# Performance work log

Hardware: AMD Instinct MI355X
Metric: run time of the kernel (lower is better)

The kernel has to match this reference:

```python
import jax, jax.numpy as jnp
import numpy as np

G = 8          # grid_size
N = G * G      # 64 nodes
DEG = 17       # neighbors per node for 8x8 sudoku (2x4 boxes)
STEPS = 32
H = 96         # hidden_dim
E = 16         # embed_size
B = 16         # batch


def sudoku_edges():
    # row (7) + col (7) + 2x4 box (7) neighbors, set-union -> 17 per node
    idx = np.arange(N).reshape(G, G)
    nb = []
    for j in range(N):
        r, c = j // G, j % G
        br, bc = (r // 2) * 2, (c // 4) * 4
        s = set(idx[r, :].tolist()) | set(idx[:, c].tolist()) | set(idx[br:br + 2, bc:bc + 4].flatten().tolist())
        s.discard(j)
        nb.append(sorted(s))
    return np.asarray(nb, dtype=np.int32)  # [64, 17]


def setup_inputs() -> dict:
    key = jax.random.key(0)
    ks = jax.random.split(key, 16)
    sc = 0.05
    inp = {
        "x": jax.random.randint(ks[0], (B, G, G), 0, G + 1),            # given digits, 0 = blank
        "target": jax.random.randint(ks[1], (B, G, G), 0, G) + 1,       # solutions in 1..8
        "edges": jnp.asarray(sudoku_edges()),                            # [64, 17] int32
        "digit_emb": jax.random.normal(ks[2], (G + 1, E), jnp.float32) * sc,
        "row_emb": jax.random.normal(ks[3], (G, E), jnp.float32) * sc,
        "col_emb": jax.random.normal(ks[4], (G, E), jnp.float32) * sc,
        "in0_W": jax.random.normal(ks[5], (3 * E, H), jnp.float32) * sc,
        "in0_b": jnp.zeros((H,), jnp.float32),
        "in_Ws": jax.random.normal(ks[6], (3, H, H), jnp.float32) * sc,
        "in_bs": jnp.zeros((3, H), jnp.float32),
        "msg0_W": jax.random.normal(ks[7], (2 * H, H), jnp.float32) * sc,
        "msg0_b": jnp.zeros((H,), jnp.float32),
        "msg_Ws": jax.random.normal(ks[8], (3, H, H), jnp.float32) * sc,
        "msg_bs": jnp.zeros((3, H), jnp.float32),
        "W_ih": jax.random.normal(ks[9], (2 * H, 4 * H), jnp.float32) * sc,
        "W_hh": jax.random.normal(ks[10], (H, 4 * H), jnp.float32) * sc,
        "b_ih": jnp.zeros((4 * H,), jnp.float32),
        "b_hh": jnp.zeros((4 * H,), jnp.float32),
        "pred_W": jax.random.normal(ks[11], (H, G), jnp.float32) * sc,
        "pred_b": jnp.zeros((G,), jnp.float32),
    }
    return inp


def _mlp(z, W0, b0, Ws, bs):
    # Linear -> ReLU -> Linear -> ReLU -> Linear -> ReLU -> Linear (def_MLP)
    z = jax.nn.relu(z @ W0 + b0)
    z = jax.nn.relu(z @ Ws[0] + bs[0])
    z = jax.nn.relu(z @ Ws[1] + bs[1])
    return z @ Ws[2] + bs[2]


def reference(x, target, edges, digit_emb, row_emb, col_emb,
              in0_W, in0_b, in_Ws, in_bs,
              msg0_W, msg0_b, msg_Ws, msg_bs,
              W_ih, W_hh, b_ih, b_hh, pred_W, pred_b):
    bsz = x.shape[0]
    xf = x.reshape(bsz, N)
    tgt = target.reshape(bsz, N) - 1                      # labels 0..7

    de = digit_emb[xf]                                    # [B,64,E]
    re = row_emb[jnp.repeat(jnp.arange(G), G)]            # [64,E]
    ce = col_emb[jnp.tile(jnp.arange(G), G)]              # [64,E]
    feat = jnp.concatenate([de,
                            jnp.broadcast_to(re[None], (bsz, N, E)),
                            jnp.broadcast_to(ce[None], (bsz, N, E))], axis=-1)
    xin = _mlp(feat, in0_W, in0_b, in_Ws, in_bs)          # [B,64,H]

    h0 = jnp.zeros((bsz, N, H), jnp.float32)
    s0 = jnp.zeros((bsz * N, H), jnp.float32)

    def step(carry, _):
        h, s, loss = carry
        # gather-by-edge message passing
        h_edges = h[:, edges]                                             # [B,64,17,H]
        h_self = jnp.broadcast_to(h[:, :, None, :], (bsz, N, DEG, H))
        msg = _mlp(jnp.concatenate([h_edges, h_self], -1),
                   msg0_W, msg0_b, msg_Ws, msg_bs).sum(axis=2)            # [B,64,H]
        # LSTMCell update
        lstm_in = jnp.concatenate([msg, xin], -1).reshape(bsz * N, 2 * H)
        gates = lstm_in @ W_ih + b_ih + h.reshape(bsz * N, H) @ W_hh + b_hh
        i, f, g, o = jnp.split(gates, 4, axis=-1)
        s2 = jax.nn.sigmoid(f) * s + jax.nn.sigmoid(i) * jnp.tanh(g)
        h2 = (jax.nn.sigmoid(o) * jnp.tanh(s2)).reshape(bsz, N, H)
        # per-step prediction / loss / accuracy
        logp = jax.nn.log_softmax(h2 @ pred_W + pred_b, axis=-1)          # [B,64,8]
        pred = jnp.argmax(logp, axis=-1)
        acc = jnp.mean(jnp.all(pred == tgt, axis=1).astype(jnp.float32))
        loss_n = -jnp.sum(jnp.take_along_axis(logp, tgt[..., None], -1)) / (bsz * N)
        return (h2, s2, loss + loss_n), acc

    (h, s, loss), accs = jax.lax.scan(step, (h0, s0, jnp.float32(0.0)), None, length=STEPS)
    loss = loss / STEPS
    final_pred = jnp.argmax(h @ pred_W + pred_b, axis=-1)                 # [B,64]
    return loss, accs, final_pred
```

## Files before the change

kernel.cpp:

```cpp
#include <hip/hip_runtime.h>

#define DEG 17
#define NSTEPS 32
#define HD 96
#define BB 16
#define NN 64
#define NODES (BB*NN)
#define Z1STR 80
#define Z2STR 84

#define WS_H      0
#define WS_S      98304
#define WS_U0     196608
#define WS_U1     393216
#define WS_XIN    590352
#define WS_GX     688656
#define WS_W1P    1081872
#define WS_W2P    1094160
#define WS_LOSSP  1106448
#define WS_CNTP   1114640

__global__ void wpad_kernel(const float* __restrict__ msg_Ws,
                            float* __restrict__ W1p, float* __restrict__ W2p)
{
  const int k = blockIdx.x;
  const int tid = threadIdx.x;
  const int jg = tid >> 3, jj = tid & 7;
  float v1 = 0.f, v2 = 0.f;
  if (jj < 6) {
    v1 = msg_Ws[k*96 + jg*6 + jj];
    v2 = msg_Ws[9216 + k*96 + jg*6 + jj];
  }
  W1p[k*128 + tid] = v1;
  W2p[k*128 + tid] = v2;
}

__global__ void init_kernel(
    const int* __restrict__ x,
    const float* __restrict__ digit_emb,
    const float* __restrict__ row_emb,
    const float* __restrict__ col_emb,
    const float* __restrict__ in0_W,
    const float* __restrict__ in0_b,
    const float* __restrict__ in_Ws,
    const float* __restrict__ in_bs,
    float* __restrict__ xin)
{
  const int node = blockIdx.x;
  const int j = threadIdx.x;
  const int n = node & 63;
  const int r = n >> 3, c = n & 7;
  __shared__ float feat[48];
  __shared__ float za[HD];
  __shared__ float zb[HD];
  if (j < 16)      feat[j] = digit_emb[x[node]*16 + j];
  else if (j < 32) feat[j] = row_emb[r*16 + (j-16)];
  else if (j < 48) feat[j] = col_emb[c*16 + (j-32)];
  __syncthreads();
  float a = in0_b[j];
  for (int k = 0; k < 48; ++k) a = fmaf(feat[k], in0_W[k*HD + j], a);
  za[j] = fmaxf(a, 0.f);
  __syncthreads();
  a = in_bs[j];
  for (int k = 0; k < HD; ++k) a = fmaf(za[k], in_Ws[k*HD + j], a);
  zb[j] = fmaxf(a, 0.f);
  __syncthreads();
  a = in_bs[HD + j];
  for (int k = 0; k < HD; ++k) a = fmaf(zb[k], in_Ws[9216 + k*HD + j], a);
  za[j] = fmaxf(a, 0.f);
  __syncthreads();
  a = in_bs[2*HD + j];
  for (int k = 0; k < HD; ++k) a = fmaf(za[k], in_Ws[2*9216 + k*HD + j], a);
  xin[node*HD + j] = a;
}

__global__ __launch_bounds__(384) void gx_kernel(
    const float* __restrict__ xin, const float* __restrict__ W_ih,
    const float* __restrict__ b_ih, const float* __restrict__ b_hh,
    float* __restrict__ gx)
{
  __shared__ float xs[4*HD];
  const int tid = threadIdx.x;
  const int base = blockIdx.x * 4;
  {
    const int m = tid / HD, k = tid - m*HD;
    xs[m*HD + k] = xin[(base+m)*HD + k];
  }
  __syncthreads();
  const int j = tid;
  float a0 = b_ih[j] + b_hh[j], a1 = a0, a2 = a0, a3 = a0;
  for (int k = 0; k < HD; ++k) {
    const float w = W_ih[(96+k)*384 + j];
    a0 = fmaf(xs[k], w, a0);
    a1 = fmaf(xs[HD+k], w, a1);
    a2 = fmaf(xs[2*HD+k], w, a2);
    a3 = fmaf(xs[3*HD+k], w, a3);
  }
  gx[(base+0)*384 + j] = a0;
  gx[(base+1)*384 + j] = a1;
  gx[(base+2)*384 + j] = a2;
  gx[(base+3)*384 + j] = a3;
}

__global__ __launch_bounds__(384) void step_kernel(
    const float* __restrict__ u_prev, float* __restrict__ u_next,
    float* __restrict__ h, float* __restrict__ s,
    const float* __restrict__ gx,
    const int* __restrict__ edges,
    const float* __restrict__ W1p, const float* __restrict__ W2p,
    const float* __restrict__ msg0_W, const float* __restrict__ msg0_b,
    const float* __restrict__ msg_Ws, const float* __restrict__ msg_bs,
    const float* __restrict__ W_ih, const float* __restrict__ W_hh,
    const float* __restrict__ pred_W, const float* __restrict__ pred_b,
    const int* __restrict__ target,
    float* __restrict__ lossP, int* __restrict__ cntP,
    float* __restrict__ final_pred_out, int step)
{
  __shared__ float sm[15744];
  float* const z1s = sm;
  float* const z2s = sm + 7680;
  float* const s3t   = sm;
  float* const msgh  = sm + 384;
  float* const h2t   = sm + 1152;
  float* const lgt   = sm + 1536;
  float* const gates = sm + 1568;
  float* const P3    = sm + 3104;
  float* const PL = z2s;
  float* const PU = z2s;

  const int tid = threadIdx.x;
  const int blk = blockIdx.x;
  const int base = blk * 4;
  const int bb = blk >> 4;
  const int nbase = (blk & 15) * 4;

  {
    const int m = tid / HD, k = tid - m*HD;
    const float usv = u_prev[(base+m)*192 + 96 + k];
    const float b0v = msg0_b[k];
    z1s[k*Z1STR + m*20 + 17] = 0.f;
    z1s[k*Z1STR + m*20 + 18] = 0.f;
    z1s[k*Z1STR + m*20 + 19] = 0.f;
    const int erow = (nbase + m) * DEG;
    #pragma unroll 1
    for (int r = 0; r < DEG; ++r) {
      const int nbr = edges[erow + r];
      const float ue = u_prev[(bb*64 + nbr)*192 + k];
      z1s[k*Z1STR + m*20 + r] = fmaxf(ue + usv + b0v, 0.f);
    }
  }
  __syncthreads();

  if (tid < 320) {
    const int jg = tid & 15, dg = tid >> 4;
    const int j6 = jg*6, j8 = jg*8, dg4 = dg*4;
    float acc[4][6];
    #pragma unroll
    for (int dd = 0; dd < 4; ++dd)
      #pragma unroll
      for (int jj = 0; jj < 6; ++jj) acc[dd][jj] = 0.f;
    #pragma unroll 4
    for (int k = 0; k < HD; ++k) {
      const float4 z = *(const float4*)&z1s[k*Z1STR + dg4];
      const float* wp = W1p + k*128 + j8;
      const float4 wa = *(const float4*)wp;
      const float2 wb = *(const float2*)(wp + 4);
      const float ze[4] = {z.x, z.y, z.z, z.w};
      const float we[6] = {wa.x, wa.y, wa.z, wa.w, wb.x, wb.y};
      #pragma unroll
      for (int dd = 0; dd < 4; ++dd)
        #pragma unroll
        for (int jj = 0; jj < 6; ++jj)
          acc[dd][jj] = fmaf(ze[dd], we[jj], acc[dd][jj]);
    }
    #pragma unroll
    for (int jj = 0; jj < 6; ++jj) {
      const float b1 = msg_bs[j6 + jj];
      float4 q;
      q.x = fmaxf(acc[0][jj] + b1, 0.f);
      q.y = fmaxf(acc[1][jj] + b1, 0.f);
      q.z = fmaxf(acc[2][jj] + b1, 0.f);
      q.w = fmaxf(acc[3][jj] + b1, 0.f);
      *(float4*)&z2s[(j6+jj)*Z2STR + dg4] = q;
    }
  }
  __syncthreads();

  {
    s3t[tid] = 0.f;
    const int m = tid / HD, k = tid - m*HD;
    msgh[(96+k)*4 + m] = h[(base+m)*HD + k];
  }
  __syncthreads();

  if (tid < 320) {
    const int jg = tid & 15, dg = tid >> 4;
    const int j6 = jg*6, j8 = jg*8, dg4 = dg*4;
    const int nd = dg / 5, dgl = dg - nd*5;
    float acc[4][6];
    #pragma unroll
    for (int dd = 0; dd < 4; ++dd)
      #pragma unroll
      for (int jj = 0; jj < 6; ++jj) acc[dd][jj] = 0.f;
    #pragma unroll 4
    for (int k = 0; k < HD; ++k) {
      const float4 z = *(const float4*)&z2s[k*Z2STR + dg4];
      const float* wp = W2p + k*128 + j8;
      const float4 wa = *(const float4*)wp;
      const float2 wb = *(const float2*)(wp + 4);
      const float ze[4] = {z.x, z.y, z.z, z.w};
      const float we[6] = {wa.x, wa.y, wa.z, wa.w, wb.x, wb.y};
      #pragma unroll
      for (int dd = 0; dd < 4; ++dd)
        #pragma unroll
        for (int jj = 0; jj < 6; ++jj)
          acc[dd][jj] = fmaf(ze[dd], we[jj], acc[dd][jj]);
    }
    const int nvalid = (dgl < 4) ? 4 : 1;
    #pragma unroll
    for (int jj = 0; jj < 6; ++jj) {
      const float b2 = msg_bs[96 + j6 + jj];
      float p = 0.f;
      #pragma unroll
      for (int dd = 0; dd < 4; ++dd)
        if (dd < nvalid) p += fmaxf(acc[dd][jj] + b2, 0.f);
      atomicAdd(&s3t[(j6+jj)*4 + nd], p);
    }
  }
  __syncthreads();

  if (tid < 192) {
    const int jg = tid % 24, kq = tid / 24;
    const int j4 = jg*4, k0 = kq*12;
    const float* W3 = msg_Ws + 2*9216;
    float acc[4][4];
    #pragma unroll
    for (int m = 0; m < 4; ++m)
      #pragma unroll
      for (int jj = 0; jj < 4; ++jj) acc[m][jj] = 0.f;
    #pragma unroll 4
    for (int kk = 0; kk < 12; ++kk) {
      const int k = k0 + kk;
      const float4 sv = *(const float4*)&s3t[k*4];
      const float4 wv = *(const float4*)&W3[k*96 + j4];
      const float se[4] = {sv.x, sv.y, sv.z, sv.w};
      const float we[4] = {wv.x, wv.y, wv.z, wv.w};
      #pragma unroll
      for (int m = 0; m < 4; ++m)
        #pragma unroll
        for (int jj = 0; jj < 4; ++jj)
          acc[m][jj] = fmaf(se[m], we[jj], acc[m][jj]);
    }
    #pragma unroll
    for (int m = 0; m < 4; ++m) {
      float4 q = {acc[m][0], acc[m][1], acc[m][2], acc[m][3]};
      *(float4*)&P3[(kq*4 + m)*96 + j4] = q;
    }
  }
  __syncthreads();
  {
    const int m = tid / HD, j = tid - m*HD;
    float v = 17.f * msg_bs[192 + j];
    #pragma unroll
    for (int kq = 0; kq < 8; ++kq) v += P3[(kq*4 + m)*96 + j];
    msgh[j*4 + m] = v;
  }
  __syncthreads();

  if (tid < 192) {
    const int jg = tid % 48, kq = tid / 48;
    const int j8 = jg*8, k0 = kq*48;
    const float* Wb = (kq < 2) ? (W_ih + j8) : (W_hh + j8 - 96*384);
    float acc[4][8];
    #pragma unroll
    for (int m = 0; m < 4; ++m)
      #pragma unroll
      for (int jj = 0; jj < 8; ++jj) acc[m][jj] = 0.f;
    #pragma unroll 2
    for (int k = k0; k < k0 + 48; ++k) {
      const float4 iv = *(const float4*)&msgh[k*4];
      const float* wp = Wb + k*384;
      const float4 wa = *(const float4*)wp;
      const float4 wc = *(const float4*)(wp + 4);
      const float ie[4] = {iv.x, iv.y, iv.z, iv.w};
      const float we[8] = {wa.x, wa.y, wa.z, wa.w, wc.x, wc.y, wc.z, wc.w};
      #pragma unroll
      for (int m = 0; m < 4; ++m)
        #pragma unroll
        for (int jj = 0; jj < 8; ++jj)
          acc[m][jj] = fmaf(ie[m], we[jj], acc[m][jj]);
    }
    #pragma unroll
    for (int m = 0; m < 4; ++m) {
      float4 qa = {acc[m][0], acc[m][1], acc[m][2], acc[m][3]};
      float4 qb = {acc[m][4], acc[m][5], acc[m][6], acc[m][7]};
      *(float4*)&PL[(kq*4 + m)*384 + j8] = qa;
      *(float4*)&PL[(kq*4 + m)*384 + j8 + 4] = qb;
    }
  }
  __syncthreads();
  {
    const int j = tid;
    #pragma unroll
    for (int m = 0; m < 4; ++m) {
      float g = gx[(base+m)*384 + j];
      #pragma unroll
      for (int kq = 0; kq < 4; ++kq) g += PL[(kq*4 + m)*384 + j];
      gates[m*384 + j] = g;
    }
  }
  __syncthreads();

  {
    const int m = tid / HD, hj = tid - m*HD;
    const int node = base + m;
    const float gi = gates[m*384 + hj];
    const float gf = gates[m*384 + 96 + hj];
    const float gg = gates[m*384 + 192 + hj];
    const float go = gates[m*384 + 288 + hj];
    const float sv = s[node*HD + hj];
    const float ig = 1.f/(1.f + expf(-gi));
    const float fg = 1.f/(1.f + expf(-gf));
    const float cg = tanhf(gg);
    const float og = 1.f/(1.f + expf(-go));
    const float s2 = fg*sv + ig*cg;
    const float h2 = og*tanhf(s2);
    s[node*HD + hj] = s2;
    h[node*HD + hj] = h2;
    h2t[hj*4 + m] = h2;
  }
  __syncthreads();

  if (tid < 192) {
    const int jg = tid % 24, kq = tid / 24;
    const int j8 = jg*8, k0 = kq*12;
    const float* Wb = (j8 < 96) ? (msg0_W + j8) : (msg0_W + 9216 + j8 - 96);
    float acc[4][8];
    #pragma unroll
    for (int m = 0; m < 4; ++m)
      #pragma unroll
      for (int jj = 0; jj < 8; ++jj) acc[m][jj] = 0.f;
    #pragma unroll 4
    for (int kk = 0; kk < 12; ++kk) {
      const int k = k0 + kk;
      const float4 iv = *(const float4*)&h2t[k*4];
      const float* wp = Wb + k*96;
      const float4 wa = *(const float4*)wp;
      const float4 wc = *(const float4*)(wp + 4);
      const float ie[4] = {iv.x, iv.y, iv.z, iv.w};
      const float we[8] = {wa.x, wa.y, wa.z, wa.w, wc.x, wc.y, wc.z, wc.w};
      #pragma unroll
      for (int m = 0; m < 4; ++m)
        #pragma unroll
        for (int jj = 0; jj < 8; ++jj)
          acc[m][jj] = fmaf(ie[m], we[jj], acc[m][jj]);
    }
    #pragma unroll
    for (int m = 0; m < 4; ++m) {
      float4 qa = {acc[m][0], acc[m][1], acc[m][2], acc[m][3]};
      float4 qb = {acc[m][4], acc[m][5], acc[m][6], acc[m][7]};
      *(float4*)&PU[(kq*4 + m)*192 + j8] = qa;
      *(float4*)&PU[(kq*4 + m)*192 + j8 + 4] = qb;
    }
  }
  __syncthreads();
  {
    const int j = tid % 192, mh = tid / 192;
    #pragma unroll
    for (int t = 0; t < 2; ++t) {
      const int mm = mh + 2*t;
      float v = 0.f;
      #pragma unroll
      for (int kq = 0; kq < 8; ++kq) v += PU[(kq*4 + mm)*192 + j];
      u_next[(base+mm)*192 + j] = v;
    }
  }

  if (tid < 256) {
    const int m = tid >> 6, c = (tid >> 3) & 7, kq = tid & 7;
    float p = 0.f;
    #pragma unroll
    for (int kk = 0; kk < 12; ++kk) {
      const int k = kq*12 + kk;
      p = fmaf(h2t[k*4 + m], pred_W[k*8 + c], p);
    }
    p += __shfl_xor(p, 1);
    p += __shfl_xor(p, 2);
    p += __shfl_xor(p, 4);
    if (kq == 0) lgt[m*8 + c] = p + pred_b[c];
  }
  __syncthreads();
  if (tid < 4) {
    const int m = tid;
    const int node = base + m;
    float mx = lgt[m*8];
    int pred = 0;
    #pragma unroll
    for (int c = 1; c < 8; ++c) {
      const float v = lgt[m*8 + c];
      if (v > mx) { mx = v; pred = c; }
    }
    float sum = 0.f;
    #pragma unroll
    for (int c = 0; c < 8; ++c) sum += expf(lgt[m*8 + c] - mx);
    const float lse = mx + logf(sum);
    const int tgt = target[node] - 1;
    lgt[16 + m] = lse - lgt[m*8 + tgt];
    lgt[20 + m] = (pred == tgt) ? 1.f : 0.f;
    if (step == NSTEPS-1) final_pred_out[node] = (float)pred;
    if (m == 0) {
      lossP[step*256 + blk] = lgt[16] + lgt[17] + lgt[18] + lgt[19];
      cntP[step*256 + blk] = (int)(lgt[20] + lgt[21] + lgt[22] + lgt[23]);
    }
  }
}

__global__ void finalize_kernel(const float* __restrict__ lossP,
                                const int* __restrict__ cntP,
                                float* __restrict__ out)
{
  __shared__ float sl[32];
  const int tid = threadIdx.x;
  const int st = tid >> 3, q = tid & 7;
  float lsum = 0.f;
  for (int i = 0; i < 32; ++i) lsum += lossP[st*256 + q*32 + i];
  lsum += __shfl_xor(lsum, 1);
  lsum += __shfl_xor(lsum, 2);
  lsum += __shfl_xor(lsum, 4);
  if (q == 0) sl[st] = lsum;
  float okc = 0.f;
  #pragma unroll
  for (int t = 0; t < 2; ++t) {
    const int bbat = q + 8*t;
    int c = 0;
    for (int i = 0; i < 16; ++i) c += cntP[st*256 + bbat*16 + i];
    okc += (c == 64) ? 1.f : 0.f;
  }
  okc += __shfl_xor(okc, 1);
  okc += __shfl_xor(okc, 2);
  okc += __shfl_xor(okc, 4);
  if (q == 0) out[1 + st] = okc / 16.f;
  __syncthreads();
  if (tid == 0) {
    float tot = 0.f;
    for (int i = 0; i < 32; ++i) tot += sl[i];
    out[0] = tot / ((float)NODES * (float)NSTEPS);
  }
}

extern "C" void kernel_launch(void* const* d_in, const int* in_sizes, int n_in,
                              void* d_out, int out_size, void* d_ws, size_t ws_size,
                              hipStream_t stream) {
  const int*   x         = (const int*)  d_in[0];
  const int*   target    = (const int*)  d_in[1];
  const int*   edges     = (const int*)  d_in[2];
  const float* digit_emb = (const float*)d_in[3];
  const float* row_emb   = (const float*)d_in[4];
  const float* col_emb   = (const float*)d_in[5];
  const float* in0_W     = (const float*)d_in[6];
  const float* in0_b     = (const float*)d_in[7];
  const float* in_Ws     = (const float*)d_in[8];
  const float* in_bs     = (const float*)d_in[9];
  const float* msg0_W    = (const float*)d_in[10];
  const float* msg0_b    = (const float*)d_in[11];
  const float* msg_Ws    = (const float*)d_in[12];
  const float* msg_bs    = (const float*)d_in[13];
  const float* W_ih      = (const float*)d_in[14];
  const float* W_hh      = (const float*)d_in[15];
  const float* pred_W    = (const float*)d_in[18];
  const float* pred_b    = (const float*)d_in[19];

  float* ws    = (float*)d_ws;
  float* hbuf  = ws + WS_H;
  float* sbuf  = ws + WS_S;
  float* u0    = ws + WS_U0;
  float* u1    = ws + WS_U1;
  float* xin   = ws + WS_XIN;
  float* gxb   = ws + WS_GX;
  float* W1p   = ws + WS_W1P;
  float* W2p   = ws + WS_W2P;
  float* lossP = ws + WS_LOSSP;
  int*   cntP  = (int*)(ws + WS_CNTP);

  hipMemsetAsync(d_ws, 0, (size_t)393216*sizeof(float), stream);

  wpad_kernel<<<96, 128, 0, stream>>>(msg_Ws, W1p, W2p);
  init_kernel<<<NODES, HD, 0, stream>>>(x, digit_emb, row_emb, col_emb,
                                        in0_W, in0_b, in_Ws, in_bs, xin);
  gx_kernel<<<256, 384, 0, stream>>>(xin, W_ih,
                                     (const float*)d_in[16], (const float*)d_in[17],
                                     gxb);

  float* outp = (float*)d_out;
  for (int st = 0; st < NSTEPS; ++st) {
    const float* up = (st & 1) ? u1 : u0;
    float*       un = (st & 1) ? u0 : u1;
    step_kernel<<<256, 384, 0, stream>>>(
        up, un, hbuf, sbuf, gxb, edges,
        W1p, W2p, msg0_W, msg0_b, msg_Ws, msg_bs,
        W_ih, W_hh, pred_W, pred_b,
        target, lossP, cntP, outp + 1 + NSTEPS, st);
  }

  finalize_kernel<<<1, 256, 0, stream>>>(lossP, cntP, outp);
}
```

Before: 1.172 ms.

## Halve nodes per block to launch 512 step blocks with smaller shared memory

```diff
diff --git a/kernel.cpp b/kernel.cpp
--- a/kernel.cpp
+++ b/kernel.cpp
@@ -3,11 +3,10 @@
 #define DEG 17
 #define NSTEPS 32
 #define HD 96
-#define BB 16
-#define NN 64
-#define NODES (BB*NN)
-#define Z1STR 80
-#define Z2STR 84
+#define NODES 1024
+#define NBLK 512
+#define Z1STR 40
+#define Z2STR 44
 
 #define WS_H      0
 #define WS_S      98304
@@ -18,7 +17,7 @@
 #define WS_W1P    1081872
 #define WS_W2P    1094160
 #define WS_LOSSP  1106448
-#define WS_CNTP   1114640
+#define WS_CNTP   (WS_LOSSP+16384)
 
 __global__ void wpad_kernel(const float* __restrict__ msg_Ws,
                             float* __restrict__ W1p, float* __restrict__ W2p)
@@ -102,7 +101,7 @@
   gx[(base+3)*384 + j] = a3;
 }
 
-__global__ __launch_bounds__(384) void step_kernel(
+__global__ __launch_bounds__(384, 3) void step_kernel(
     const float* __restrict__ u_prev, float* __restrict__ u_next,
     float* __restrict__ h, float* __restrict__ s,
     const float* __restrict__ gx,
@@ -116,203 +115,213 @@
     float* __restrict__ lossP, int* __restrict__ cntP,
     float* __restrict__ final_pred_out, int step)
 {
-  __shared__ float sm[15744];
+  __shared__ float sm[8064];
   float* const z1s = sm;
-  float* const z2s = sm + 7680;
+  float* const z2s = sm + 3840;
   float* const s3t   = sm;
-  float* const msgh  = sm + 384;
-  float* const h2t   = sm + 1152;
-  float* const lgt   = sm + 1536;
-  float* const gates = sm + 1568;
-  float* const P3    = sm + 3104;
+  float* const msgh  = sm + 192;
+  float* const h2t   = sm + 576;
+  float* const lgt   = sm + 768;
+  float* const gates = sm + 800;
+  float* const P2    = sm + 1568;
+  float* const P3 = z2s;
   float* const PL = z2s;
   float* const PU = z2s;
 
   const int tid = threadIdx.x;
   const int blk = blockIdx.x;
-  const int base = blk * 4;
-  const int bb = blk >> 4;
-  const int nbase = (blk & 15) * 4;
-
-  {
-    const int m = tid / HD, k = tid - m*HD;
-    const float usv = u_prev[(base+m)*192 + 96 + k];
-    const float b0v = msg0_b[k];
-    z1s[k*Z1STR + m*20 + 17] = 0.f;
-    z1s[k*Z1STR + m*20 + 18] = 0.f;
-    z1s[k*Z1STR + m*20 + 19] = 0.f;
-    const int erow = (nbase + m) * DEG;
-    #pragma unroll 1
-    for (int r = 0; r < DEG; ++r) {
-      const int nbr = edges[erow + r];
-      const float ue = u_prev[(bb*64 + nbr)*192 + k];
-      z1s[k*Z1STR + m*20 + r] = fmaxf(ue + usv + b0v, 0.f);
+  const int base = blk * 2;
+  const int bb = blk >> 5;
+  const int nbase = (blk & 31) * 2;
+
+  if (tid < 320) {
+    const int row = tid % 40;
+    const int kq  = tid / 40;
+    const int k0 = kq*12;
+    const int m = row / 20, r = row - m*20;
+    if (r < 17) {
+      const int nbr = edges[(nbase + m)*DEG + r];
+      const float* upe = u_prev + (bb*64 + nbr)*192 + k0;
+      const float* ups = u_prev + (base+m)*192 + 96 + k0;
+      const float* b0p = msg0_b + k0;
+      #pragma unroll
+      for (int t = 0; t < 3; ++t) {
+        const float4 ue = *(const float4*)(upe + t*4);
+        const float4 us = *(const float4*)(ups + t*4);
+        const float4 b0 = *(const float4*)(b0p + t*4);
+        z1s[(k0+t*4+0)*Z1STR + row] = fmaxf(ue.x+us.x+b0.x, 0.f);
+        z1s[(k0+t*4+1)*Z1STR + row] = fmaxf(ue.y+us.y+b0.y, 0.f);
+        z1s[(k0+t*4+2)*Z1STR + row] = fmaxf(ue.z+us.z+b0.z, 0.f);
+        z1s[(k0+t*4+3)*Z1STR + row] = fmaxf(ue.w+us.w+b0.w, 0.f);
+      }
+    } else {
+      #pragma unroll
+      for (int t = 0; t < 12; ++t) z1s[(k0+t)*Z1STR + row] = 0.f;
     }
   }
   __syncthreads();
 
   if (tid < 320) {
     const int jg = tid & 15, dg = tid >> 4;
-    const int j6 = jg*6, j8 = jg*8, dg4 = dg*4;
-    float acc[4][6];
-    #pragma unroll
-    for (int dd = 0; dd < 4; ++dd)
+    const int j6 = jg*6, j8 = jg*8, d2 = dg*2;
+    float acc[2][6];
+    #pragma unroll
+    for (int dd = 0; dd < 2; ++dd)
       #pragma unroll
       for (int jj = 0; jj < 6; ++jj) acc[dd][jj] = 0.f;
     #pragma unroll 4
     for (int k = 0; k < HD; ++k) {
-      const float4 z = *(const float4*)&z1s[k*Z1STR + dg4];
+      const float2 z = *(const float2*)&z1s[k*Z1STR + d2];
       const float* wp = W1p + k*128 + j8;
       const float4 wa = *(const float4*)wp;
       const float2 wb = *(const float2*)(wp + 4);
-      const float ze[4] = {z.x, z.y, z.z, z.w};
       const float we[6] = {wa.x, wa.y, wa.z, wa.w, wb.x, wb.y};
       #pragma unroll
-      for (int dd = 0; dd < 4; ++dd)
-        #pragma unroll
-        for (int jj = 0; jj < 6; ++jj)
-          acc[dd][jj] = fmaf(ze[dd], we[jj], acc[dd][jj]);
+      for (int jj = 0; jj < 6; ++jj) {
+        acc[0][jj] = fmaf(z.x, we[jj], acc[0][jj]);
+        acc[1][jj] = fmaf(z.y, we[jj], acc[1][jj]);
+      }
     }
     #pragma unroll
     for (int jj = 0; jj < 6; ++jj) {
       const float b1 = msg_bs[j6 + jj];
-      float4 q;
+      float2 q;
       q.x = fmaxf(acc[0][jj] + b1, 0.f);
       q.y = fmaxf(acc[1][jj] + b1, 0.f);
-      q.z = fmaxf(acc[2][jj] + b1, 0.f);
-      q.w = fmaxf(acc[3][jj] + b1, 0.f);
-      *(float4*)&z2s[(j6+jj)*Z2STR + dg4] = q;
-    }
-  }
-  __syncthreads();
-
-  {
-    s3t[tid] = 0.f;
-    const int m = tid / HD, k = tid - m*HD;
-    msgh[(96+k)*4 + m] = h[(base+m)*HD + k];
+      *(float2*)&z2s[(j6+jj)*Z2STR + d2] = q;
+    }
   }
   __syncthreads();
 
   if (tid < 320) {
     const int jg = tid & 15, dg = tid >> 4;
-    const int j6 = jg*6, j8 = jg*8, dg4 = dg*4;
-    const int nd = dg / 5, dgl = dg - nd*5;
-    float acc[4][6];
-    #pragma unroll
-    for (int dd = 0; dd < 4; ++dd)
+    const int j6 = jg*6, j8 = jg*8, d2 = dg*2;
+    const int rl = (dg % 10) * 2;
+    float acc[2][6];
+    #pragma unroll
+    for (int dd = 0; dd < 2; ++dd)
       #pragma unroll
       for (int jj = 0; jj < 6; ++jj) acc[dd][jj] = 0.f;
     #pragma unroll 4
     for (int k = 0; k < HD; ++k) {
-      const float4 z = *(const float4*)&z2s[k*Z2STR + dg4];
+      const float2 z = *(const float2*)&z2s[k*Z2STR + d2];
       const float* wp = W2p + k*128 + j8;
       const float4 wa = *(const float4*)wp;
       const float2 wb = *(const float2*)(wp + 4);
-      const float ze[4] = {z.x, z.y, z.z, z.w};
       const float we[6] = {wa.x, wa.y, wa.z, wa.w, wb.x, wb.y};
       #pragma unroll
-      for (int dd = 0; dd < 4; ++dd)
-        #pragma unroll
-        for (int jj = 0; jj < 6; ++jj)
-          acc[dd][jj] = fmaf(ze[dd], we[jj], acc[dd][jj]);
-    }
-    const int nvalid = (dgl < 4) ? 4 : 1;
+      for (int jj = 0; jj < 6; ++jj) {
+        acc[0][jj] = fmaf(z.x, we[jj], acc[0][jj]);
+        acc[1][jj] = fmaf(z.y, we[jj], acc[1][jj]);
+      }
+    }
+    const bool v0 = (rl <= 16), v1 = (rl < 16);
     #pragma unroll
     for (int jj = 0; jj < 6; ++jj) {
       const float b2 = msg_bs[96 + j6 + jj];
       float p = 0.f;
-      #pragma unroll
-      for (int dd = 0; dd < 4; ++dd)
-        if (dd < nvalid) p += fmaxf(acc[dd][jj] + b2, 0.f);
-      atomicAdd(&s3t[(j6+jj)*4 + nd], p);
+      if (v0) p += fmaxf(acc[0][jj] + b2, 0.f);
+      if (v1) p += fmaxf(acc[1][jj] + b2, 0.f);
+      P2[(j6+jj)*20 + dg] = p;
+    }
+  } else {
+    const int idx = tid - 320;
+    #pragma unroll
+    for (int t = 0; t < 3; ++t) {
+      const int e = idx + 64*t;
+      const int m = e / 96, k = e - m*96;
+      msgh[(96+k)*2 + m] = h[(base+m)*HD + k];
     }
   }
   __syncthreads();
 
   if (tid < 192) {
-    const int jg = tid % 24, kq = tid / 24;
-    const int j4 = jg*4, k0 = kq*12;
+    const int m = tid / 96, j = tid - m*96;
+    float v = 0.f;
+    #pragma unroll
+    for (int d = 0; d < 10; ++d) v += P2[j*20 + m*10 + d];
+    s3t[j*2 + m] = v;
+  }
+  __syncthreads();
+
+  {
+    const int j4g = tid % 24, kq = tid / 24;
+    const int j4 = j4g*4, k0 = kq*6;
     const float* W3 = msg_Ws + 2*9216;
-    float acc[4][4];
-    #pragma unroll
-    for (int m = 0; m < 4; ++m)
+    float acc[2][4];
+    #pragma unroll
+    for (int m = 0; m < 2; ++m)
       #pragma unroll
       for (int jj = 0; jj < 4; ++jj) acc[m][jj] = 0.f;
-    #pragma unroll 4
-    for (int kk = 0; kk < 12; ++kk) {
+    #pragma unroll
+    for (int kk = 0; kk < 6; ++kk) {
       const int k = k0 + kk;
-      const float4 sv = *(const float4*)&s3t[k*4];
+      const float2 sv = *(const float2*)&s3t[k*2];
       const float4 wv = *(const float4*)&W3[k*96 + j4];
-      const float se[4] = {sv.x, sv.y, sv.z, sv.w};
       const float we[4] = {wv.x, wv.y, wv.z, wv.w};
       #pragma unroll
-      for (int m = 0; m < 4; ++m)
-        #pragma unroll
-        for (int jj = 0; jj < 4; ++jj)
-          acc[m][jj] = fmaf(se[m], we[jj], acc[m][jj]);
-    }
-    #pragma unroll
-    for (int m = 0; m < 4; ++m) {
+      for (int jj = 0; jj < 4; ++jj) {
+        acc[0][jj] = fmaf(sv.x, we[jj], acc[0][jj]);
+        acc[1][jj] = fmaf(sv.y, we[jj], acc[1][jj]);
+      }
+    }
+    #pragma unroll
+    for (int m = 0; m < 2; ++m) {
       float4 q = {acc[m][0], acc[m][1], acc[m][2], acc[m][3]};
-      *(float4*)&P3[(kq*4 + m)*96 + j4] = q;
-    }
-  }
-  __syncthreads();
+      *(float4*)&P3[kq*192 + m*96 + j4] = q;
+    }
+  }
+  __syncthreads();
+  if (tid < 192) {
+    const int m = tid / 96, j = tid - m*96;
+    float v = 17.f * msg_bs[192 + j];
+    #pragma unroll
+    for (int kq = 0; kq < 16; ++kq) v += P3[kq*192 + m*96 + j];
+    msgh[j*2 + m] = v;
+  }
+  __syncthreads();
+
   {
-    const int m = tid / HD, j = tid - m*HD;
-    float v = 17.f * msg_bs[192 + j];
-    #pragma unroll
-    for (int kq = 0; kq < 8; ++kq) v += P3[(kq*4 + m)*96 + j];
-    msgh[j*4 + m] = v;
-  }
-  __syncthreads();
-
-  if (tid < 192) {
-    const int jg = tid % 48, kq = tid / 48;
-    const int j8 = jg*8, k0 = kq*48;
-    const float* Wb = (kq < 2) ? (W_ih + j8) : (W_hh + j8 - 96*384);
-    float acc[4][8];
-    #pragma unroll
-    for (int m = 0; m < 4; ++m)
-      #pragma unroll
-      for (int jj = 0; jj < 8; ++jj) acc[m][jj] = 0.f;
+    const int jg = tid % 96, kq = tid / 96;
+    const int j4 = jg*4, k0 = kq*48;
+    const float* Wp = (kq < 2) ? (W_ih + k0*384) : (W_hh + (k0-96)*384);
+    float acc[2][4];
+    #pragma unroll
+    for (int m = 0; m < 2; ++m)
+      #pragma unroll
+      for (int jj = 0; jj < 4; ++jj) acc[m][jj] = 0.f;
     #pragma unroll 2
-    for (int k = k0; k < k0 + 48; ++k) {
-      const float4 iv = *(const float4*)&msgh[k*4];
-      const float* wp = Wb + k*384;
-      const float4 wa = *(const float4*)wp;
-      const float4 wc = *(const float4*)(wp + 4);
-      const float ie[4] = {iv.x, iv.y, iv.z, iv.w};
-      const float we[8] = {wa.x, wa.y, wa.z, wa.w, wc.x, wc.y, wc.z, wc.w};
-      #pragma unroll
-      for (int m = 0; m < 4; ++m)
-        #pragma unroll
-        for (int jj = 0; jj < 8; ++jj)
-          acc[m][jj] = fmaf(ie[m], we[jj], acc[m][jj]);
-    }
-    #pragma unroll
-    for (int m = 0; m < 4; ++m) {
-      float4 qa = {acc[m][0], acc[m][1], acc[m][2], acc[m][3]};
-      float4 qb = {acc[m][4], acc[m][5], acc[m][6], acc[m][7]};
-      *(float4*)&PL[(kq*4 + m)*384 + j8] = qa;
-      *(float4*)&PL[(kq*4 + m)*384 + j8 + 4] = qb;
+    for (int kk = 0; kk < 48; ++kk) {
+      const float2 iv = *(const float2*)&msgh[(k0+kk)*2];
+      const float4 wv = *(const float4*)&Wp[kk*384 + j4];
+      const float we[4] = {wv.x, wv.y, wv.z, wv.w};
+      #pragma unroll
+      for (int jj = 0; jj < 4; ++jj) {
+        acc[0][jj] = fmaf(iv.x, we[jj], acc[0][jj]);
+        acc[1][jj] = fmaf(iv.y, we[jj], acc[1][jj]);
+      }
+    }
+    #pragma unroll
+    for (int m = 0; m < 2; ++m) {
+      float4 q = {acc[m][0], acc[m][1], acc[m][2], acc[m][3]};
+      *(float4*)&PL[kq*768 + m*384 + j4] = q;
     }
   }
   __syncthreads();
   {
     const int j = tid;
     #pragma unroll
-    for (int m = 0; m < 4; ++m) {
+    for (int m = 0; m < 2; ++m) {
       float g = gx[(base+m)*384 + j];
       #pragma unroll
-      for (int kq = 0; kq < 4; ++kq) g += PL[(kq*4 + m)*384 + j];
+      for (int kq = 0; kq < 4; ++kq) g += PL[kq*768 + m*384 + j];
       gates[m*384 + j] = g;
     }
   }
   __syncthreads();
 
-  {
-    const int m = tid / HD, hj = tid - m*HD;
+  if (tid < 192) {
+    const int m = tid / 96, hj = tid - m*96;
     const int node = base + m;
     const float gi = gates[m*384 + hj];
     const float gf = gates[m*384 + 96 + hj];
@@ -327,62 +336,53 @@
     const float h2 = og*tanhf(s2);
     s[node*HD + hj] = s2;
     h[node*HD + hj] = h2;
-    h2t[hj*4 + m] = h2;
-  }
-  __syncthreads();
-
-  if (tid < 192) {
-    const int jg = tid % 24, kq = tid / 24;
-    const int j8 = jg*8, k0 = kq*12;
-    const float* Wb = (j8 < 96) ? (msg0_W + j8) : (msg0_W + 9216 + j8 - 96);
-    float acc[4][8];
-    #pragma unroll
-    for (int m = 0; m < 4; ++m)
-      #pragma unroll
-      for (int jj = 0; jj < 8; ++jj) acc[m][jj] = 0.f;
+    h2t[hj*2 + m] = h2;
+  }
+  __syncthreads();
+
+  {
+    const int jg = tid % 48, kq = tid / 48;
+    const int j4 = jg*4, k0 = kq*12;
+    const float* Wp = (j4 < 96) ? (msg0_W + j4) : (msg0_W + 9216 + j4 - 96);
+    float acc[2][4];
+    #pragma unroll
+    for (int m = 0; m < 2; ++m)
+      #pragma unroll
+      for (int jj = 0; jj < 4; ++jj) acc[m][jj] = 0.f;
     #pragma unroll 4
     for (int kk = 0; kk < 12; ++kk) {
       const int k = k0 + kk;
-      const float4 iv = *(const float4*)&h2t[k*4];
-      const float* wp = Wb + k*96;
-      const float4 wa = *(const float4*)wp;
-      const float4 wc = *(const float4*)(wp + 4);
-      const float ie[4] = {iv.x, iv.y, iv.z, iv.w};
-      const float we[8] = {wa.x, wa.y, wa.z, wa.w, wc.x, wc.y, wc.z, wc.w};
-      #pragma unroll
-      for (int m = 0; m < 4; ++m)
-        #pragma unroll
-        for (int jj = 0; jj < 8; ++jj)
-          acc[m][jj] = fmaf(ie[m], we[jj], acc[m][jj]);
-    }
-    #pragma unroll
-    for (int m = 0; m < 4; ++m) {
-      float4 qa = {acc[m][0], acc[m][1], acc[m][2], acc[m][3]};
-      float4 qb = {acc[m][4], acc[m][5], acc[m][6], acc[m][7]};
-      *(float4*)&PU[(kq*4 + m)*192 + j8] = qa;
-      *(float4*)&PU[(kq*4 + m)*192 + j8 + 4] = qb;
-    }
-  }
-  __syncthreads();
+      const float2 iv = *(const float2*)&h2t[k*2];
+      const float4 wv = *(const float4*)&Wp[k*96];
+      const float we[4] = {wv.x, wv.y, wv.z, wv.w};
+      #pragma unroll
+      for (int jj = 0; jj < 4; ++jj) {
+        acc[0][jj] = fmaf(iv.x, we[jj], acc[0][jj]);
+        acc[1][jj] = fmaf(iv.y, we[jj], acc[1][jj]);
+      }
+    }
+    #pragma unroll
+    for (int m = 0; m < 2; ++m) {
+      float4 q = {acc[m][0], acc[m][1], acc[m][2], acc[m][3]};
+      *(float4*)&PU[kq*384 + m*192 + j4] = q;
+    }
+  }
+  __syncthreads();
+
   {
-    const int j = tid % 192, mh = tid / 192;
-    #pragma unroll
-    for (int t = 0; t < 2; ++t) {
-      const int mm = mh + 2*t;
-      float v = 0.f;
-      #pragma unroll
-      for (int kq = 0; kq < 8; ++kq) v += PU[(kq*4 + mm)*192 + j];
-      u_next[(base+mm)*192 + j] = v;
-    }
-  }
-
-  if (tid < 256) {
+    const int j = tid % 192, m = tid / 192;
+    float v = 0.f;
+    #pragma unroll
+    for (int kq = 0; kq < 8; ++kq) v += PU[kq*384 + m*192 + j];
+    u_next[(base+m)*192 + j] = v;
+  }
+  if (tid < 128) {
     const int m = tid >> 6, c = (tid >> 3) & 7, kq = tid & 7;
     float p = 0.f;
     #pragma unroll
     for (int kk = 0; kk < 12; ++kk) {
       const int k = kq*12 + kk;
-      p = fmaf(h2t[k*4 + m], pred_W[k*8 + c], p);
+      p = fmaf(h2t[k*2 + m], pred_W[k*8 + c], p);
     }
     p += __shfl_xor(p, 1);
     p += __shfl_xor(p, 2);
@@ -390,7 +390,8 @@
     if (kq == 0) lgt[m*8 + c] = p + pred_b[c];
   }
   __syncthreads();
-  if (tid < 4) {
+
+  if (tid < 2) {
     const int m = tid;
     const int node = base + m;
     float mx = lgt[m*8];
@@ -406,11 +407,11 @@
     const float lse = mx + logf(sum);
     const int tgt = target[node] - 1;
     lgt[16 + m] = lse - lgt[m*8 + tgt];
-    lgt[20 + m] = (pred == tgt) ? 1.f : 0.f;
+    lgt[18 + m] = (pred == tgt) ? 1.f : 0.f;
     if (step == NSTEPS-1) final_pred_out[node] = (float)pred;
     if (m == 0) {
-      lossP[step*256 + blk] = lgt[16] + lgt[17] + lgt[18] + lgt[19];
-      cntP[step*256 + blk] = (int)(lgt[20] + lgt[21] + lgt[22] + lgt[23]);
+      lossP[step*NBLK + blk] = lgt[16] + lgt[17];
+      cntP[step*NBLK + blk] = (int)(lgt[18] + lgt[19]);
     }
   }
 }
@@ -423,7 +424,7 @@
   const int tid = threadIdx.x;
   const int st = tid >> 3, q = tid & 7;
   float lsum = 0.f;
-  for (int i = 0; i < 32; ++i) lsum += lossP[st*256 + q*32 + i];
+  for (int i = 0; i < 64; ++i) lsum += lossP[st*NBLK + q*64 + i];
   lsum += __shfl_xor(lsum, 1);
   lsum += __shfl_xor(lsum, 2);
   lsum += __shfl_xor(lsum, 4);
@@ -433,7 +434,7 @@
   for (int t = 0; t < 2; ++t) {
     const int bbat = q + 8*t;
     int c = 0;
-    for (int i = 0; i < 16; ++i) c += cntP[st*256 + bbat*16 + i];
+    for (int i = 0; i < 32; ++i) c += cntP[st*NBLK + bbat*32 + i];
     okc += (c == 64) ? 1.f : 0.f;
   }
   okc += __shfl_xor(okc, 1);
@@ -495,7 +496,7 @@
   for (int st = 0; st < NSTEPS; ++st) {
     const float* up = (st & 1) ? u1 : u0;
     float*       un = (st & 1) ? u0 : u1;
-    step_kernel<<<256, 384, 0, stream>>>(
+    step_kernel<<<NBLK, 384, 0, stream>>>(
         up, un, hbuf, sbuf, gxb, edges,
         W1p, W2p, msg0_W, msg0_b, msg_Ws, msg_bs,
         W_ih, W_hh, pred_W, pred_b,
```

After: 1.485 ms. 1.27x slower.
